# Kernel tuning notes

Hardware: AMD Instinct MI355X
Metric: run time of the kernel (lower is better)

The kernel has to match this reference:

```python
import jax, jax.numpy as jnp
import numpy as np

B, N, M, D = 8, 4096, 4096, 3

def setup_inputs() -> dict:
    key = jax.random.key(0)
    ks = jax.random.split(key, 6)
    return {
        "X_pred": jax.random.normal(ks[0], (B, N, D), dtype=jnp.float32),
        "X_true": jax.random.normal(ks[1], (B, M, D), dtype=jnp.float32),
        "R_pred": jax.random.normal(ks[2], (B, D, D), dtype=jnp.float32),
        "t_pred": jax.random.normal(ks[3], (B, D), dtype=jnp.float32),
        "R_true": jax.random.normal(ks[4], (B, D, D), dtype=jnp.float32),
        "t_true": jax.random.normal(ks[5], (B, D), dtype=jnp.float32),
        "temperature": jnp.asarray(0.1, dtype=jnp.float32),
    }

def reference(X_pred, X_true, R_pred, t_pred, R_true, t_true, temperature):
    # Rigid transforms: x' = R x + t
    Xp = jnp.einsum('bij,bnj->bni', R_pred, X_pred) + t_pred[:, None, :]  # (B,N,D)
    Xt = jnp.einsum('bij,bmj->bmi', R_true, X_true) + t_true[:, None, :]  # (B,M,D)
    # Squared pairwise distances: |a|^2 + |b|^2 - 2 a.b  (== cdist(p=2)**2)
    sq_p = jnp.sum(Xp * Xp, axis=-1)  # (B,N)
    sq_t = jnp.sum(Xt * Xt, axis=-1)  # (B,M)
    dist_sq = sq_p[:, :, None] + sq_t[:, None, :] - 2.0 * jnp.einsum('bnd,bmd->bnm', Xp, Xt)
    dist_sq = jnp.maximum(dist_sq, 0.0)  # (B,N,M)
    soft_alignment = jax.nn.softmax(-dist_sq / temperature, axis=-1)
    weighted_distances = jnp.sum(soft_alignment * dist_sq, axis=-1)  # (B,N)
    return jnp.mean(weighted_distances)
```

## Files before the change

kernel.cpp:

```cpp
#include <hip/hip_runtime.h>


#define B_    8
#define N_    4096
#define M_    4096
#define NWAVE 8
#define BLOCK (NWAVE * 64)
#define ROWS  256
#define MSPL  8
#define QCH   (M_ / MSPL)
#define WQ    (QCH / NWAVE)
#define LOG2E 1.4426950408889634f
#define LN2   0.6931471805599453f
#define BIGF  3.0e38f

__global__ __launch_bounds__(BLOCK, 8) void softfape_main(
    const float* __restrict__ X_pred, const float* __restrict__ X_true,
    const float* __restrict__ R_pred, const float* __restrict__ t_pred,
    const float* __restrict__ R_true, const float* __restrict__ t_true,
    const float* __restrict__ temp,
    float4* __restrict__ Pg)
{
    __shared__ float4 Q[QCH];
    __shared__ float  Mp[NWAVE][ROWS];
    __shared__ float  Lp[NWAVE][ROWS];
    __shared__ float  Sp[NWAVE][ROWS];
    __shared__ float  shl[ROWS];
    __shared__ float  pwl[ROWS];

    const int tid  = threadIdx.x;
    const int wave = tid >> 6;
    const int lane = tid & 63;
    const int x    = blockIdx.x;
    const int ms   = x & 7;
    const int rg   = (x >> 3) & 15;
    const int b    = x >> 7;

    const float T   = temp[0];
    const float c   = LOG2E / T;
    const float m2c = -2.0f * c;

    if (tid < QCH / 2) {
        const float g00 = R_true[b*9+0], g01 = R_true[b*9+1], g02 = R_true[b*9+2];
        const float g10 = R_true[b*9+3], g11 = R_true[b*9+4], g12 = R_true[b*9+5];
        const float g20 = R_true[b*9+6], g21 = R_true[b*9+7], g22 = R_true[b*9+8];
        const float u0  = t_true[b*3+0], u1 = t_true[b*3+1], u2 = t_true[b*3+2];
        const float2* xt = (const float2*)(X_true + ((size_t)b * M_ + ms * QCH) * 3);
        const float2 f0 = xt[3*tid+0], f1 = xt[3*tid+1], f2 = xt[3*tid+2];
        {
            const float y0 = fmaf(g00, f0.x, fmaf(g01, f0.y, fmaf(g02, f1.x, u0)));
            const float y1 = fmaf(g10, f0.x, fmaf(g11, f0.y, fmaf(g12, f1.x, u1)));
            const float y2 = fmaf(g20, f0.x, fmaf(g21, f0.y, fmaf(g22, f1.x, u2)));
            const float nn = fmaf(y0, y0, fmaf(y1, y1, y2 * y2));
            Q[2*tid]   = make_float4(m2c*y0, m2c*y1, m2c*y2, c*nn);
        }
        {
            const float y0 = fmaf(g00, f1.y, fmaf(g01, f2.x, fmaf(g02, f2.y, u0)));
            const float y1 = fmaf(g10, f1.y, fmaf(g11, f2.x, fmaf(g12, f2.y, u1)));
            const float y2 = fmaf(g20, f1.y, fmaf(g21, f2.x, fmaf(g22, f2.y, u2)));
            const float nn = fmaf(y0, y0, fmaf(y1, y1, y2 * y2));
            Q[2*tid+1] = make_float4(m2c*y0, m2c*y1, m2c*y2, c*nn);
        }
    }

    float px[4], py[4], pz[4], pw[4];
    {
        const float h00 = R_pred[b*9+0], h01 = R_pred[b*9+1], h02 = R_pred[b*9+2];
        const float h10 = R_pred[b*9+3], h11 = R_pred[b*9+4], h12 = R_pred[b*9+5];
        const float h20 = R_pred[b*9+6], h21 = R_pred[b*9+7], h22 = R_pred[b*9+8];
        const float v0 = t_pred[b*3+0], v1 = t_pred[b*3+1], v2 = t_pred[b*3+2];
        const float4* xp = (const float4*)(X_pred + ((size_t)b * N_ + rg * ROWS + lane * 4) * 3);
        const float4 a0 = xp[0], a1 = xp[1], a2 = xp[2];
        const float rx[4] = {a0.x, a0.w, a1.z, a2.y};
        const float ry[4] = {a0.y, a1.x, a1.w, a2.z};
        const float rz[4] = {a0.z, a1.y, a2.x, a2.w};
        #pragma unroll
        for (int r = 0; r < 4; ++r) {
            px[r] = fmaf(h00, rx[r], fmaf(h01, ry[r], fmaf(h02, rz[r], v0)));
            py[r] = fmaf(h10, rx[r], fmaf(h11, ry[r], fmaf(h12, rz[r], v1)));
            pz[r] = fmaf(h20, rx[r], fmaf(h21, ry[r], fmaf(h22, rz[r], v2)));
            pw[r] = c * fmaf(px[r], px[r], fmaf(py[r], py[r], pz[r] * pz[r]));
            pwl[4*lane + r] = pw[r];
        }
    }

    __syncthreads();

    const float4* __restrict__ Qw = Q + wave * WQ;

    float mA[4] = {BIGF, BIGF, BIGF, BIGF};
    #pragma unroll 8
    for (int k = 0; k < WQ; ++k) {
        const float4 q = Qw[k];
        #pragma unroll
        for (int r = 0; r < 4; ++r) {
            const float A = fmaf(q.x, px[r], fmaf(q.y, py[r], fmaf(q.z, pz[r], q.w)));
            mA[r] = fminf(mA[r], A);
        }
    }
    #pragma unroll
    for (int r = 0; r < 4; ++r) Mp[wave][4*lane + r] = mA[r];
    __syncthreads();

    if (tid < ROWS) {
        float m = Mp[0][tid];
        #pragma unroll
        for (int w2 = 1; w2 < NWAVE; ++w2) m = fminf(m, Mp[w2][tid]);
        shl[tid] = m;
    }
    __syncthreads();

    const float4 sh4 = *(const float4*)&shl[4*lane];
    const float sh[4] = {sh4.x, sh4.y, sh4.z, sh4.w};

    float L[4]  = {0.f, 0.f, 0.f, 0.f};
    float SA[4] = {0.f, 0.f, 0.f, 0.f};
    #pragma unroll 8
    for (int k = 0; k < WQ; ++k) {
        const float4 q = Qw[k];
        #pragma unroll
        for (int r = 0; r < 4; ++r) {
            const float A   = fmaf(q.x, px[r], fmaf(q.y, py[r], fmaf(q.z, pz[r], q.w)));
            const float arg = sh[r] - A;
            const float w   = __builtin_amdgcn_exp2f(arg);
            L[r] += w;
            SA[r] = fmaf(w, arg, SA[r]);
        }
    }
    #pragma unroll
    for (int r = 0; r < 4; ++r) {
        Lp[wave][4*lane + r] = L[r];
        Sp[wave][4*lane + r] = SA[r];
    }
    __syncthreads();

    if (tid < ROWS) {
        float Lr = 0.0f, Sr = 0.0f;
        #pragma unroll
        for (int w2 = 0; w2 < NWAVE; ++w2) { Lr += Lp[w2][tid]; Sr += Sp[w2][tid]; }
        const size_t row = (size_t)b * N_ + rg * ROWS + tid;
        Pg[row * MSPL + ms] = make_float4(shl[tid] + pwl[tid], Lr, Sr, 0.0f);
    }
}

__global__ __launch_bounds__(256) void softfape_finalize(
    const float4* __restrict__ Pg, const float* __restrict__ temp,
    float* __restrict__ out)
{
    __shared__ float ws4[4];
    const int tid = threadIdx.x;
    const size_t row = (size_t)blockIdx.x * 256 + tid;

    float4 P[MSPL];
    #pragma unroll
    for (int i = 0; i < MSPL; ++i) P[i] = Pg[row * MSPL + i];

    float m = P[0].x;
    #pragma unroll
    for (int i = 1; i < MSPL; ++i) m = fminf(m, P[i].x);

    float L = 0.0f, SA = 0.0f;
    #pragma unroll
    for (int i = 0; i < MSPL; ++i) {
        const float dm = m - P[i].x;
        const float f  = __builtin_amdgcn_exp2f(dm);
        L  = fmaf(P[i].y, f, L);
        SA = fmaf(f, fmaf(dm, P[i].y, P[i].z), SA);
    }
    float wd = m - SA / L;

    wd += __shfl_xor(wd, 1);  wd += __shfl_xor(wd, 2);  wd += __shfl_xor(wd, 4);
    wd += __shfl_xor(wd, 8);  wd += __shfl_xor(wd, 16); wd += __shfl_xor(wd, 32);
    if ((tid & 63) == 0) ws4[tid >> 6] = wd;
    __syncthreads();
    if (tid == 0) {
        const float s = ws4[0] + ws4[1] + ws4[2] + ws4[3];
        const float scale = temp[0] * LN2 / ((float)B_ * (float)N_);
        atomicAdd(out, s * scale);
    }
}

extern "C" void kernel_launch(void* const* d_in, const int* in_sizes, int n_in,
                              void* d_out, int out_size, void* d_ws, size_t ws_size,
                              hipStream_t stream) {
    const float* X_pred = (const float*)d_in[0];
    const float* X_true = (const float*)d_in[1];
    const float* R_pred = (const float*)d_in[2];
    const float* t_pred = (const float*)d_in[3];
    const float* R_true = (const float*)d_in[4];
    const float* t_true = (const float*)d_in[5];
    const float* temp   = (const float*)d_in[6];
    float* out = (float*)d_out;

    float4* Pg = (float4*)d_ws;

    hipMemsetAsync(out, 0, sizeof(float), stream);

    softfape_main<<<dim3(B_ * 16 * MSPL), BLOCK, 0, stream>>>(
        X_pred, X_true, R_pred, t_pred, R_true, t_true, temp, Pg);

    softfape_finalize<<<dim3((B_ * N_) / 256), 256, 0, stream>>>(Pg, temp, out);
}
```

Measured before the change: 102.6 us.

## Double rows per thread and use packed float2 math in softmax loops

```diff
diff --git a/kernel.cpp b/kernel.cpp
--- a/kernel.cpp
+++ b/kernel.cpp
@@ -6,7 +6,7 @@
 #define M_    4096
 #define NWAVE 8
 #define BLOCK (NWAVE * 64)
-#define ROWS  256
+#define ROWS  512
 #define MSPL  8
 #define QCH   (M_ / MSPL)
 #define WQ    (QCH / NWAVE)
@@ -14,7 +14,9 @@
 #define LN2   0.6931471805599453f
 #define BIGF  3.0e38f
 
-__global__ __launch_bounds__(BLOCK, 8) void softfape_main(
+typedef float v2f __attribute__((ext_vector_type(2)));
+
+__global__ __launch_bounds__(BLOCK, 6) void softfape_main(
     const float* __restrict__ X_pred, const float* __restrict__ X_true,
     const float* __restrict__ R_pred, const float* __restrict__ t_pred,
     const float* __restrict__ R_true, const float* __restrict__ t_true,
@@ -22,8 +24,7 @@
     float4* __restrict__ Pg)
 {
     __shared__ float4 Q[QCH];
-    __shared__ float  Mp[NWAVE][ROWS];
-    __shared__ float  Lp[NWAVE][ROWS];
+    __shared__ float  MLp[NWAVE][ROWS];
     __shared__ float  Sp[NWAVE][ROWS];
     __shared__ float  shl[ROWS];
     __shared__ float  pwl[ROWS];
@@ -33,8 +34,8 @@
     const int lane = tid & 63;
     const int x    = blockIdx.x;
     const int ms   = x & 7;
-    const int rg   = (x >> 3) & 15;
-    const int b    = x >> 7;
+    const int rg   = (x >> 3) & 7;
+    const int b    = x >> 6;
 
     const float T   = temp[0];
     const float c   = LOG2E / T;
@@ -63,24 +64,27 @@
         }
     }
 
-    float px[4], py[4], pz[4], pw[4];
+    v2f px2[4], py2[4], pz2[4];
     {
         const float h00 = R_pred[b*9+0], h01 = R_pred[b*9+1], h02 = R_pred[b*9+2];
         const float h10 = R_pred[b*9+3], h11 = R_pred[b*9+4], h12 = R_pred[b*9+5];
         const float h20 = R_pred[b*9+6], h21 = R_pred[b*9+7], h22 = R_pred[b*9+8];
         const float v0 = t_pred[b*3+0], v1 = t_pred[b*3+1], v2 = t_pred[b*3+2];
-        const float4* xp = (const float4*)(X_pred + ((size_t)b * N_ + rg * ROWS + lane * 4) * 3);
+        const float4* xp = (const float4*)(X_pred + ((size_t)b * N_ + rg * ROWS + lane * 8) * 3);
         const float4 a0 = xp[0], a1 = xp[1], a2 = xp[2];
-        const float rx[4] = {a0.x, a0.w, a1.z, a2.y};
-        const float ry[4] = {a0.y, a1.x, a1.w, a2.z};
-        const float rz[4] = {a0.z, a1.y, a2.x, a2.w};
-        #pragma unroll
-        for (int r = 0; r < 4; ++r) {
-            px[r] = fmaf(h00, rx[r], fmaf(h01, ry[r], fmaf(h02, rz[r], v0)));
-            py[r] = fmaf(h10, rx[r], fmaf(h11, ry[r], fmaf(h12, rz[r], v1)));
-            pz[r] = fmaf(h20, rx[r], fmaf(h21, ry[r], fmaf(h22, rz[r], v2)));
-            pw[r] = c * fmaf(px[r], px[r], fmaf(py[r], py[r], pz[r] * pz[r]));
-            pwl[4*lane + r] = pw[r];
+        const float4 a3 = xp[3], a4 = xp[4], a5 = xp[5];
+        const float rx[8] = {a0.x, a0.w, a1.z, a2.y, a3.x, a3.w, a4.z, a5.y};
+        const float ry[8] = {a0.y, a1.x, a1.w, a2.z, a3.y, a4.x, a4.w, a5.z};
+        const float rz[8] = {a0.z, a1.y, a2.x, a2.w, a3.z, a4.y, a5.x, a5.w};
+        #pragma unroll
+        for (int j = 0; j < 8; ++j) {
+            const float ppx = fmaf(h00, rx[j], fmaf(h01, ry[j], fmaf(h02, rz[j], v0)));
+            const float ppy = fmaf(h10, rx[j], fmaf(h11, ry[j], fmaf(h12, rz[j], v1)));
+            const float ppz = fmaf(h20, rx[j], fmaf(h21, ry[j], fmaf(h22, rz[j], v2)));
+            px2[j >> 1][j & 1] = ppx;
+            py2[j >> 1][j & 1] = ppy;
+            pz2[j >> 1][j & 1] = ppz;
+            pwl[8*lane + j] = c * fmaf(ppx, ppx, fmaf(ppy, ppy, ppz * ppz));
         }
     }
 
@@ -88,56 +92,69 @@
 
     const float4* __restrict__ Qw = Q + wave * WQ;
 
-    float mA[4] = {BIGF, BIGF, BIGF, BIGF};
-    #pragma unroll 8
+    v2f mA2[4] = {{BIGF, BIGF}, {BIGF, BIGF}, {BIGF, BIGF}, {BIGF, BIGF}};
+    #pragma unroll 4
     for (int k = 0; k < WQ; ++k) {
         const float4 q = Qw[k];
-        #pragma unroll
-        for (int r = 0; r < 4; ++r) {
-            const float A = fmaf(q.x, px[r], fmaf(q.y, py[r], fmaf(q.z, pz[r], q.w)));
-            mA[r] = fminf(mA[r], A);
-        }
-    }
-    #pragma unroll
-    for (int r = 0; r < 4; ++r) Mp[wave][4*lane + r] = mA[r];
-    __syncthreads();
-
-    if (tid < ROWS) {
-        float m = Mp[0][tid];
-        #pragma unroll
-        for (int w2 = 1; w2 < NWAVE; ++w2) m = fminf(m, Mp[w2][tid]);
+        const v2f qx = {q.x, q.x}, qy = {q.y, q.y}, qz = {q.z, q.z}, qw = {q.w, q.w};
+        #pragma unroll
+        for (int j = 0; j < 4; ++j) {
+            const v2f A = qx * px2[j] + (qy * py2[j] + (qz * pz2[j] + qw));
+            mA2[j] = __builtin_elementwise_min(mA2[j], A);
+        }
+    }
+    #pragma unroll
+    for (int j = 0; j < 4; ++j) {
+        MLp[wave][8*lane + 2*j]     = mA2[j].x;
+        MLp[wave][8*lane + 2*j + 1] = mA2[j].y;
+    }
+    __syncthreads();
+
+    {
+        float m = MLp[0][tid];
+        #pragma unroll
+        for (int w2 = 1; w2 < NWAVE; ++w2) m = fminf(m, MLp[w2][tid]);
         shl[tid] = m;
     }
     __syncthreads();
 
-    const float4 sh4 = *(const float4*)&shl[4*lane];
-    const float sh[4] = {sh4.x, sh4.y, sh4.z, sh4.w};
-
-    float L[4]  = {0.f, 0.f, 0.f, 0.f};
-    float SA[4] = {0.f, 0.f, 0.f, 0.f};
-    #pragma unroll 8
+    v2f sh2[4];
+    {
+        const float4 s0 = *(const float4*)&shl[8*lane];
+        const float4 s1 = *(const float4*)&shl[8*lane + 4];
+        sh2[0] = (v2f){s0.x, s0.y};  sh2[1] = (v2f){s0.z, s0.w};
+        sh2[2] = (v2f){s1.x, s1.y};  sh2[3] = (v2f){s1.z, s1.w};
+    }
+
+    v2f L2[4]  = {{0.f,0.f},{0.f,0.f},{0.f,0.f},{0.f,0.f}};
+    v2f SA2[4] = {{0.f,0.f},{0.f,0.f},{0.f,0.f},{0.f,0.f}};
+    #pragma unroll 4
     for (int k = 0; k < WQ; ++k) {
         const float4 q = Qw[k];
-        #pragma unroll
-        for (int r = 0; r < 4; ++r) {
-            const float A   = fmaf(q.x, px[r], fmaf(q.y, py[r], fmaf(q.z, pz[r], q.w)));
-            const float arg = sh[r] - A;
-            const float w   = __builtin_amdgcn_exp2f(arg);
-            L[r] += w;
-            SA[r] = fmaf(w, arg, SA[r]);
-        }
-    }
-    #pragma unroll
-    for (int r = 0; r < 4; ++r) {
-        Lp[wave][4*lane + r] = L[r];
-        Sp[wave][4*lane + r] = SA[r];
-    }
-    __syncthreads();
-
-    if (tid < ROWS) {
+        const v2f qx = {q.x, q.x}, qy = {q.y, q.y}, qz = {q.z, q.z}, qw = {q.w, q.w};
+        #pragma unroll
+        for (int j = 0; j < 4; ++j) {
+            const v2f A   = qx * px2[j] + (qy * py2[j] + (qz * pz2[j] + qw));
+            const v2f arg = sh2[j] - A;
+            const v2f w   = {__builtin_amdgcn_exp2f(arg.x),
+                             __builtin_amdgcn_exp2f(arg.y)};
+            L2[j]  += w;
+            SA2[j]  = w * arg + SA2[j];
+        }
+    }
+    #pragma unroll
+    for (int j = 0; j < 4; ++j) {
+        MLp[wave][8*lane + 2*j]     = L2[j].x;
+        MLp[wave][8*lane + 2*j + 1] = L2[j].y;
+        Sp[wave][8*lane + 2*j]      = SA2[j].x;
+        Sp[wave][8*lane + 2*j + 1]  = SA2[j].y;
+    }
+    __syncthreads();
+
+    {
         float Lr = 0.0f, Sr = 0.0f;
         #pragma unroll
-        for (int w2 = 0; w2 < NWAVE; ++w2) { Lr += Lp[w2][tid]; Sr += Sp[w2][tid]; }
+        for (int w2 = 0; w2 < NWAVE; ++w2) { Lr += MLp[w2][tid]; Sr += Sp[w2][tid]; }
         const size_t row = (size_t)b * N_ + rg * ROWS + tid;
         Pg[row * MSPL + ms] = make_float4(shl[tid] + pwl[tid], Lr, Sr, 0.0f);
     }
@@ -196,7 +213,7 @@
 
     hipMemsetAsync(out, 0, sizeof(float), stream);
 
-    softfape_main<<<dim3(B_ * 16 * MSPL), BLOCK, 0, stream>>>(
+    softfape_main<<<dim3(B_ * 8 * MSPL), BLOCK, 0, stream>>>(
         X_pred, X_true, R_pred, t_pred, R_true, t_true, temp, Pg);
 
     softfape_finalize<<<dim3((B_ * N_) / 256), 256, 0, stream>>>(Pg, temp, out);
```

Result: slower. 105.3 us (+2.7%).
